# Kernel tuning notes

Measured on AMD Instinct MI355X. Metric: run time of the kernel, lower is better.

## Reference

```python
import jax, jax.numpy as jnp
import numpy as np

B, S, NX, NH = 2, 2048, 1024, 16
HD = NX // NH  # head dim = 64

def setup_inputs() -> dict:
    key = jax.random.key(0)
    k1, k2, k3 = jax.random.split(key, 3)
    return {
        "x": jax.random.normal(k1, (B, S, NX), dtype=jnp.float32),
        "c_attn_w": jax.random.normal(k2, (NX, 3 * NX), dtype=jnp.float32) * 0.02,
        "c_attn_b": jnp.zeros((3 * NX,), dtype=jnp.float32),
        "c_proj_w": jax.random.normal(k3, (NX, NX), dtype=jnp.float32) * 0.02,
        "c_proj_b": jnp.zeros((NX,), dtype=jnp.float32),
    }

def reference(x, c_attn_w, c_attn_b, c_proj_w, c_proj_b):
    b, s, nx = x.shape
    # fused QKV projection (Conv1D == affine on last dim)
    qkv = x @ c_attn_w + c_attn_b                      # [b, s, 3*nx]
    q, k, v = jnp.split(qkv, 3, axis=-1)
    # split heads -> [b, h, s, d]
    q = q.reshape(b, s, NH, HD).transpose(0, 2, 1, 3)
    k = k.reshape(b, s, NH, HD).transpose(0, 2, 1, 3)
    v = v.reshape(b, s, NH, HD).transpose(0, 2, 1, 3)
    # scaled scores with causal mask (masked_fill -1e10, matching original)
    w = jnp.einsum("bhqd,bhkd->bhqk", q, k) / jnp.sqrt(jnp.float32(HD))
    causal = jnp.tril(jnp.ones((s, s), dtype=bool))    # [s, s]
    w = jnp.where(causal[None, None, :, :], w, jnp.float32(-1e10))
    w = jax.nn.softmax(w, axis=-1)
    a = jnp.einsum("bhqk,bhkd->bhqd", w, v)            # [b, h, s, d]
    # merge heads
    a = a.transpose(0, 2, 1, 3).reshape(b, s, nx)
    # output projection (dropout is identity in eval)
    return a @ c_proj_w + c_proj_b
```

## Files before the change

kernel.cpp:

```cpp
#include <hip/hip_runtime.h>
#include <cstdint>

typedef unsigned short u16;
typedef unsigned int u32;
typedef float f32x4 __attribute__((ext_vector_type(4)));
typedef __bf16 bf16x8 __attribute__((ext_vector_type(8)));
typedef __bf16 bf16x4 __attribute__((ext_vector_type(4)));
typedef u16 u16x8 __attribute__((ext_vector_type(8)));

#define B_ 2
#define S_ 2048
#define NX_ 1024
#define NH_ 16
#define HD_ 64
#define T3_ 3072
#define M_ 4096
#define SCL 0.18033688011112042f

__device__ __forceinline__ u16 bfbits(float f) {
    __bf16 h = (__bf16)f;
    return __builtin_bit_cast(u16, h);
}

__device__ __forceinline__ void gload_lds16(const void* g, void* l) {
    auto gp = reinterpret_cast<const __attribute__((address_space(1))) u32*>(
        reinterpret_cast<uintptr_t>(g));
    auto lp = reinterpret_cast<__attribute__((address_space(3))) u32*>(
        reinterpret_cast<uintptr_t>(l));
    __builtin_amdgcn_global_load_lds(gp, lp, 16, 0, 0);
}

__global__ __launch_bounds__(256) void cvt_bf16_kernel(const float* __restrict__ X,
                                                       u16* __restrict__ Y) {
    int i = (blockIdx.x * 256 + threadIdx.x) * 4;
    float4 v = *reinterpret_cast<const float4*>(X + i);
    bf16x4 o;
    o[0] = (__bf16)v.x; o[1] = (__bf16)v.y; o[2] = (__bf16)v.z; o[3] = (__bf16)v.w;
    *reinterpret_cast<bf16x4*>(Y + i) = o;
}

__global__ __launch_bounds__(256) void transpose_cvt_kernel(const float* __restrict__ W,
                                                            u16* __restrict__ WT,
                                                            int K, int N) {
    __shared__ float tile[32][33];
    int nbx = N >> 5;
    int nb = (blockIdx.x % nbx) << 5;
    int kb = (blockIdx.x / nbx) << 5;
    int tx = threadIdx.x & 31, ty = threadIdx.x >> 5;
#pragma unroll
    for (int i = 0; i < 32; i += 8)
        tile[ty + i][tx] = W[(size_t)(kb + ty + i) * N + nb + tx];
    __syncthreads();
#pragma unroll
    for (int i = 0; i < 32; i += 8)
        WT[(size_t)(nb + ty + i) * K + kb + tx] = bfbits(tile[tx][ty + i]);
}

#define BM 128
#define BN 128
#define BK 64
__global__ __launch_bounds__(256) void gemm_bt_kernel(const u16* __restrict__ A,
                                                      const u16* __restrict__ Bt,
                                                      const float* __restrict__ bias,
                                                      u16* __restrict__ Cb,
                                                      float* __restrict__ Cf,
                                                      u16* __restrict__ Vt,
                                                      int vcol0, int qcols,
                                                      int M, int N, int K) {
    __shared__ u16 a_lds[2][BM * BK];
    __shared__ u16 b_lds[2][BN * BK];
    int nbn = N / BN;
    int nwg = gridDim.x;
    int orig = blockIdx.x;
    int wg = (orig & 7) * (nwg >> 3) + (orig >> 3);
    int bm = wg / nbn, bn = wg % nbn;
    int t = threadIdx.x;
    int w = t >> 6, l = t & 63, lg = l >> 4, lr = l & 15;
    int wr = w >> 1, wc = w & 1;
    const u16* Abase = A + (size_t)bm * BM * K;
    const u16* Bbase = Bt + (size_t)bn * BN * K;

    f32x4 zero4 = {0.f, 0.f, 0.f, 0.f};
    f32x4 acc[4][4];
#pragma unroll
    for (int m = 0; m < 4; ++m)
#pragma unroll
        for (int n = 0; n < 4; ++n) acc[m][n] = zero4;

    auto stage = [&](int kt, int bs) {
#pragma unroll
        for (int it = 0; it < 4; ++it) {
            int idx = it * 256 + t;
            int row = idx >> 3, ck = idx & 7;
            int cds = ck ^ (row & 7);
            int ubase = (it * 256 + w * 64) * 8;
            gload_lds16(Abase + (size_t)row * K + kt * BK + cds * 8, &a_lds[bs][ubase]);
            gload_lds16(Bbase + (size_t)row * K + kt * BK + cds * 8, &b_lds[bs][ubase]);
        }
    };

    stage(0, 0);
    __syncthreads();

    int nkt = K / BK;
    for (int kt = 0; kt < nkt; ++kt) {
        int cur = kt & 1;
        if (kt + 1 < nkt) stage(kt + 1, cur ^ 1);

#pragma unroll
        for (int ks = 0; ks < 2; ++ks) {
            int ck = (ks * 4 + lg) ^ (lr & 7);
            bf16x8 af[4], bf[4];
#pragma unroll
            for (int m = 0; m < 4; ++m)
                af[m] = *reinterpret_cast<const bf16x8*>(
                    &a_lds[cur][(wr * 64 + m * 16 + lr) * BK + ck * 8]);
#pragma unroll
            for (int n = 0; n < 4; ++n)
                bf[n] = *reinterpret_cast<const bf16x8*>(
                    &b_lds[cur][(wc * 64 + n * 16 + lr) * BK + ck * 8]);
            __builtin_amdgcn_s_setprio(1);
#pragma unroll
            for (int m = 0; m < 4; ++m)
#pragma unroll
                for (int n = 0; n < 4; ++n)
                    acc[m][n] = __builtin_amdgcn_mfma_f32_16x16x32_bf16(
                        af[m], bf[n], acc[m][n], 0, 0, 0);
            __builtin_amdgcn_s_setprio(0);
        }
        __syncthreads();
    }

#pragma unroll
    for (int n = 0; n < 4; ++n) {
        int col0 = bn * BN + wc * 64 + n * 16;
        int col = col0 + lr;
        float bv = bias[col];
        float sc = (col0 < qcols) ? SCL : 1.0f;
        bool isv = (Vt != nullptr) && (col0 >= vcol0);
#pragma unroll
        for (int m = 0; m < 4; ++m) {
            int row0 = bm * BM + wr * 64 + m * 16 + lg * 4;
            if (isv) {
                int nv = col - vcol0, hh = nv >> 6, dd = nv & 63;
                int bb = row0 >> 11, ss = row0 & 2047;
                bf16x4 pk;
#pragma unroll
                for (int r = 0; r < 4; ++r) pk[r] = (__bf16)(acc[m][n][r] + bv);
                *reinterpret_cast<bf16x4*>(
                    Vt + (((size_t)(bb * 16 + hh) * 64 + dd) << 11) + ss) = pk;
            } else {
#pragma unroll
                for (int r = 0; r < 4; ++r) {
                    float v = (acc[m][n][r] + bv) * sc;
                    if (Cf) Cf[(size_t)(row0 + r) * N + col] = v;
                    else    Cb[(size_t)(row0 + r) * N + col] = bfbits(v);
                }
            }
        }
    }
}

__global__ __launch_bounds__(512) void attn_kernel(const u16* __restrict__ qkv,
                                                   const u16* __restrict__ Vt,
                                                   u16* __restrict__ outa) {
    __shared__ u16 k_lds[2][4096];
    __shared__ u16 v_lds[2][4096];
    __shared__ u16 p_lds[8192];

    int bid = blockIdx.x;
    int g = bid & 31;
    int j = bid >> 5;
    int qt = (j < 8) ? (15 - j) : (j - 8);
    int b = g >> 4, h = g & 15;
    int t = threadIdx.x, w = t >> 6, l = t & 63, lg = l >> 4, lr = l & 15;
    const u16* base = qkv + (size_t)b * S_ * T3_;
    const u16* vbase = Vt + (size_t)g * 64 * S_;
    int prow = w * 16 + lr;
    int qb = qt * 128;
    int qrow = qb + w * 16 + lr;

    int srow = w * 8 + (l >> 3);
    auto stage = [&](int kt2, int bs) {
        int kb2 = kt2 * 64;
        int ckg = (l & 7) ^ (srow & 7);
        gload_lds16(base + (size_t)(kb2 + srow) * T3_ + NX_ + h * 64 + ckg * 8,
                    &k_lds[bs][w * 512]);
        gload_lds16(vbase + (size_t)srow * S_ + kb2 + ckg * 8,
                    &v_lds[bs][w * 512]);
    };

    f32x4 zero4 = {0.f, 0.f, 0.f, 0.f};

    bf16x8 qf[2];
#pragma unroll
    for (int ks = 0; ks < 2; ++ks)
        qf[ks] = *reinterpret_cast<const bf16x8*>(
            base + (size_t)qrow * T3_ + h * 64 + ks * 32 + lg * 8);

    f32x4 oacc[4];
#pragma unroll
    for (int dc = 0; dc < 4; ++dc) oacc[dc] = zero4;
    float mrun = -1e30f, lrun = 0.f;
    int nkt = 2 * qt + 2;
    int tw = 2 * qt + (w >> 2);

    stage(0, 0);
    __syncthreads();

    for (int kt = 0; kt < nkt; ++kt) {
        int cur = kt & 1;
        if (kt + 1 < nkt) stage(kt + 1, cur ^ 1);

        if (kt <= tw) {
            int kb = kt * 64;
            f32x4 sacc[4];
#pragma unroll
            for (int kn = 0; kn < 4; ++kn) sacc[kn] = zero4;
            __builtin_amdgcn_s_setprio(1);
#pragma unroll
            for (int ks = 0; ks < 2; ++ks) {
#pragma unroll
                for (int kn = 0; kn < 4; ++kn) {
                    bf16x8 kf = *reinterpret_cast<const bf16x8*>(
                        &k_lds[cur][(kn * 16 + lr) * 64 + (((ks * 4 + lg) ^ (lr & 7)) * 8)]);
                    sacc[kn] = __builtin_amdgcn_mfma_f32_16x16x32_bf16(
                        kf, qf[ks], sacc[kn], 0, 0, 0);
                }
            }
            __builtin_amdgcn_s_setprio(0);

            if (kt == tw) {
#pragma unroll
                for (int kn = 0; kn < 4; ++kn)
#pragma unroll
                    for (int r = 0; r < 4; ++r)
                        if (kb + kn * 16 + lg * 4 + r > qrow) sacc[kn][r] = -1e30f;
            }

            float mx = -1e30f;
#pragma unroll
            for (int kn = 0; kn < 4; ++kn) {
                float a0 = fmaxf(sacc[kn][0], sacc[kn][1]);
                float a1 = fmaxf(sacc[kn][2], sacc[kn][3]);
                mx = fmaxf(mx, fmaxf(a0, a1));
            }
            mx = fmaxf(mx, __shfl_xor(mx, 16));
            mx = fmaxf(mx, __shfl_xor(mx, 32));

            bool noresc = __all(mx <= mrun + 1.5f);
            float mnew = noresc ? mrun : fmaxf(mrun, mx);

            float rs = 0.f;
#pragma unroll
            for (int kn = 0; kn < 4; ++kn)
#pragma unroll
                for (int r = 0; r < 4; ++r) {
                    float pv = exp2f(sacc[kn][r] - mnew);
                    sacc[kn][r] = pv;
                    rs += pv;
                }
            rs += __shfl_xor(rs, 16);
            rs += __shfl_xor(rs, 32);

            if (noresc) {
                lrun += rs;
            } else {
                float fsc = exp2f(mrun - mnew);
                mrun = mnew;
                lrun = lrun * fsc + rs;
                float f0 = __shfl(fsc, lg * 4 + 0);
                float f1 = __shfl(fsc, lg * 4 + 1);
                float f2 = __shfl(fsc, lg * 4 + 2);
                float f3 = __shfl(fsc, lg * 4 + 3);
#pragma unroll
                for (int dc = 0; dc < 4; ++dc) {
                    oacc[dc][0] *= f0; oacc[dc][1] *= f1;
                    oacc[dc][2] *= f2; oacc[dc][3] *= f3;
                }
            }

#pragma unroll
            for (int kn = 0; kn < 4; ++kn) {
                bf16x4 pb;
                pb[0] = (__bf16)sacc[kn][0]; pb[1] = (__bf16)sacc[kn][1];
                pb[2] = (__bf16)sacc[kn][2]; pb[3] = (__bf16)sacc[kn][3];
                int byteoff = prow * 128 + (((2 * kn + (lg >> 1)) ^ (prow & 7)) * 16) + (lg & 1) * 8;
                *reinterpret_cast<bf16x4*>(reinterpret_cast<char*>(p_lds) + byteoff) = pb;
            }

            __builtin_amdgcn_s_setprio(1);
#pragma unroll
            for (int ks = 0; ks < 2; ++ks) {
                bf16x8 pf = *reinterpret_cast<const bf16x8*>(
                    reinterpret_cast<char*>(p_lds) + prow * 128 + (((ks * 4 + lg) ^ (prow & 7)) * 16));
#pragma unroll
                for (int dc = 0; dc < 4; ++dc) {
                    bf16x8 vf = *reinterpret_cast<const bf16x8*>(
                        &v_lds[cur][(dc * 16 + lr) * 64 + (((ks * 4 + lg) ^ (lr & 7)) * 8)]);
                    oacc[dc] = __builtin_amdgcn_mfma_f32_16x16x32_bf16(
                        pf, vf, oacc[dc], 0, 0, 0);
                }
            }
            __builtin_amdgcn_s_setprio(0);
        }
        __syncthreads();
    }

    float inv = 1.f / lrun;
    float i0 = __shfl(inv, lg * 4 + 0);
    float i1 = __shfl(inv, lg * 4 + 1);
    float i2 = __shfl(inv, lg * 4 + 2);
    float i3 = __shfl(inv, lg * 4 + 3);
    u16* ob = outa + (size_t)b * S_ * NX_;
#pragma unroll
    for (int r = 0; r < 4; ++r) {
        float ir = (r == 0) ? i0 : (r == 1) ? i1 : (r == 2) ? i2 : i3;
        int row = qb + w * 16 + lg * 4 + r;
#pragma unroll
        for (int dc = 0; dc < 4; ++dc)
            ob[(size_t)row * NX_ + h * 64 + dc * 16 + lr] = bfbits(oacc[dc][r] * ir);
    }
}

extern "C" void kernel_launch(void* const* d_in, const int* in_sizes, int n_in,
                              void* d_out, int out_size, void* d_ws, size_t ws_size,
                              hipStream_t stream) {
    const float* x        = (const float*)d_in[0];
    const float* c_attn_w = (const float*)d_in[1];
    const float* c_attn_b = (const float*)d_in[2];
    const float* c_proj_w = (const float*)d_in[3];
    const float* c_proj_b = (const float*)d_in[4];
    float* out = (float*)d_out;

    u16* xb     = (u16*)d_ws;
    u16* wqkvT  = xb + (size_t)M_ * NX_;
    u16* wprojT = wqkvT + (size_t)T3_ * NX_;
    u16* qkv    = wprojT + (size_t)NX_ * NX_;
    u16* attno  = xb;
    u16* Vtp    = (u16*)d_out;

    cvt_bf16_kernel<<<(M_ * NX_) / 1024, 256, 0, stream>>>(x, xb);
    transpose_cvt_kernel<<<(T3_ / 32) * (NX_ / 32), 256, 0, stream>>>(c_attn_w, wqkvT, NX_, T3_);
    transpose_cvt_kernel<<<(NX_ / 32) * (NX_ / 32), 256, 0, stream>>>(c_proj_w, wprojT, NX_, NX_);
    gemm_bt_kernel<<<(M_ / BM) * (T3_ / BN), 256, 0, stream>>>(
        xb, wqkvT, c_attn_b, qkv, nullptr, Vtp, 2 * NX_, NX_, M_, T3_, NX_);
    attn_kernel<<<512, 512, 0, stream>>>(qkv, Vtp, attno);
    gemm_bt_kernel<<<(M_ / BM) * (NX_ / BN), 256, 0, stream>>>(
        attno, wprojT, c_proj_b, nullptr, out, nullptr, 0, 0, M_, NX_, NX_);
}
```

Measured before the change: 120.1 us.

## Split attention KV range across two workgroups and merge partials; XCD-aware GEMM tile mapping

Each query tile's causal key range is now split into two halves handled by separate workgroups, so the attention grid doubles to 1024 blocks. Each half writes unnormalized bf16 partial outputs plus running max and sum, and a new merge kernel rescales and combines them. The aim is more parallelism and better balance on the long causal tiles. The cost is an extra kernel launch, extra memory traffic for partials and stats, and some precision loss from storing unnormalized partials in bf16. The GEMM block-to-tile mapping is also reworked to group tiles per XCD into 2D sub-grids for cache locality.

```diff
diff --git a/kernel.cpp b/kernel.cpp
--- a/kernel.cpp
+++ b/kernel.cpp
@@ -66,14 +66,14 @@
                                                       float* __restrict__ Cf,
                                                       u16* __restrict__ Vt,
                                                       int vcol0, int qcols,
+                                                      int gx, int sbm, int sbn,
                                                       int M, int N, int K) {
     __shared__ u16 a_lds[2][BM * BK];
     __shared__ u16 b_lds[2][BN * BK];
-    int nbn = N / BN;
-    int nwg = gridDim.x;
     int orig = blockIdx.x;
-    int wg = (orig & 7) * (nwg >> 3) + (orig >> 3);
-    int bm = wg / nbn, bn = wg % nbn;
+    int xcd = orig & 7, li = orig >> 3;
+    int bm = (xcd % gx) * sbm + li / sbn;
+    int bn = (xcd / gx) * sbn + li % sbn;
     int t = threadIdx.x;
     int w = t >> 6, l = t & 63, lg = l >> 4, lr = l & 15;
     int wr = w >> 1, wc = w & 1;
@@ -163,7 +163,9 @@
 
 __global__ __launch_bounds__(512) void attn_kernel(const u16* __restrict__ qkv,
                                                    const u16* __restrict__ Vt,
-                                                   u16* __restrict__ outa) {
+                                                   u16* __restrict__ part0,
+                                                   u16* __restrict__ part1,
+                                                   float* __restrict__ mlb) {
     __shared__ u16 k_lds[2][4096];
     __shared__ u16 v_lds[2][4096];
     __shared__ u16 p_lds[8192];
@@ -171,7 +173,8 @@
     int bid = blockIdx.x;
     int g = bid & 31;
     int j = bid >> 5;
-    int qt = (j < 8) ? (15 - j) : (j - 8);
+    int qt = 15 - (j >> 1);
+    int s = j & 1;
     int b = g >> 4, h = g & 15;
     int t = threadIdx.x, w = t >> 6, l = t & 63, lg = l >> 4, lr = l & 15;
     const u16* base = qkv + (size_t)b * S_ * T3_;
@@ -179,6 +182,10 @@
     int prow = w * 16 + lr;
     int qb = qt * 128;
     int qrow = qb + w * 16 + lr;
+
+    int tw = 2 * qt + (w >> 2);
+    int k0 = s ? (qt + 1) : 0;
+    int k1 = s ? (2 * qt + 2) : (qt + 1);
 
     int srow = w * 8 + (l >> 3);
     auto stage = [&](int kt2, int bs) {
@@ -202,15 +209,13 @@
 #pragma unroll
     for (int dc = 0; dc < 4; ++dc) oacc[dc] = zero4;
     float mrun = -1e30f, lrun = 0.f;
-    int nkt = 2 * qt + 2;
-    int tw = 2 * qt + (w >> 2);
-
-    stage(0, 0);
+
+    stage(k0, 0);
     __syncthreads();
 
-    for (int kt = 0; kt < nkt; ++kt) {
-        int cur = kt & 1;
-        if (kt + 1 < nkt) stage(kt + 1, cur ^ 1);
+    for (int kt = k0; kt < k1; ++kt) {
+        int cur = (kt - k0) & 1;
+        if (kt + 1 < k1) stage(kt + 1, cur ^ 1);
 
         if (kt <= tw) {
             int kb = kt * 64;
@@ -307,19 +312,42 @@
         __syncthreads();
     }
 
-    float inv = 1.f / lrun;
-    float i0 = __shfl(inv, lg * 4 + 0);
-    float i1 = __shfl(inv, lg * 4 + 1);
-    float i2 = __shfl(inv, lg * 4 + 2);
-    float i3 = __shfl(inv, lg * 4 + 3);
-    u16* ob = outa + (size_t)b * S_ * NX_;
+    u16* pb = (s ? part1 : part0) + (size_t)b * S_ * NX_;
 #pragma unroll
     for (int r = 0; r < 4; ++r) {
-        float ir = (r == 0) ? i0 : (r == 1) ? i1 : (r == 2) ? i2 : i3;
         int row = qb + w * 16 + lg * 4 + r;
 #pragma unroll
         for (int dc = 0; dc < 4; ++dc)
-            ob[(size_t)row * NX_ + h * 64 + dc * 16 + lr] = bfbits(oacc[dc][r] * ir);
+            pb[(size_t)row * NX_ + h * 64 + dc * 16 + lr] = bfbits(oacc[dc][r]);
+    }
+    if (lg == 0) {
+        float* f = mlb + (size_t)(b * S_ + qrow) * (T3_ / 2) + NX_ + h * 4 + s * 2;
+        f[0] = mrun; f[1] = lrun;
+    }
+}
+
+__global__ __launch_bounds__(256) void merge_kernel(u16* __restrict__ part0,
+                                                    const u16* __restrict__ part1,
+                                                    const float* __restrict__ mlb) {
+    int idx = blockIdx.x * 256 + threadIdx.x;
+    int tok = idx >> 4, h = idx & 15;
+    const float* f = mlb + (size_t)tok * (T3_ / 2) + NX_ + h * 4;
+    float m0 = f[0], l0 = f[1], m1 = f[2], l1 = f[3];
+    float M = fmaxf(m0, m1);
+    float e0 = exp2f(m0 - M), e1 = exp2f(m1 - M);
+    float inv = 1.f / (l0 * e0 + l1 * e1);
+    float a = e0 * inv, c = e1 * inv;
+    u16* p0 = part0 + (size_t)tok * NX_ + h * 64;
+    const u16* p1 = part1 + (size_t)tok * NX_ + h * 64;
+#pragma unroll
+    for (int i = 0; i < 8; ++i) {
+        bf16x8 v0 = *reinterpret_cast<const bf16x8*>(p0 + i * 8);
+        bf16x8 v1 = *reinterpret_cast<const bf16x8*>(p1 + i * 8);
+        bf16x8 o;
+#pragma unroll
+        for (int k = 0; k < 8; ++k)
+            o[k] = (__bf16)((float)v0[k] * a + (float)v1[k] * c);
+        *reinterpret_cast<bf16x8*>(p0 + i * 8) = o;
     }
 }
 
@@ -339,13 +367,16 @@
     u16* qkv    = wprojT + (size_t)NX_ * NX_;
     u16* attno  = xb;
     u16* Vtp    = (u16*)d_out;
+    u16* part1  = Vtp + (size_t)32 * 64 * S_;
+    float* mlb  = (float*)qkv;
 
     cvt_bf16_kernel<<<(M_ * NX_) / 1024, 256, 0, stream>>>(x, xb);
     transpose_cvt_kernel<<<(T3_ / 32) * (NX_ / 32), 256, 0, stream>>>(c_attn_w, wqkvT, NX_, T3_);
     transpose_cvt_kernel<<<(NX_ / 32) * (NX_ / 32), 256, 0, stream>>>(c_proj_w, wprojT, NX_, NX_);
     gemm_bt_kernel<<<(M_ / BM) * (T3_ / BN), 256, 0, stream>>>(
-        xb, wqkvT, c_attn_b, qkv, nullptr, Vtp, 2 * NX_, NX_, M_, T3_, NX_);
-    attn_kernel<<<512, 512, 0, stream>>>(qkv, Vtp, attno);
+        xb, wqkvT, c_attn_b, qkv, nullptr, Vtp, 2 * NX_, NX_, 4, 8, 12, M_, T3_, NX_);
+    attn_kernel<<<1024, 512, 0, stream>>>(qkv, Vtp, attno, part1, mlb);
+    merge_kernel<<<(M_ * NH_) / 256, 256, 0, stream>>>(attno, part1, mlb);
     gemm_bt_kernel<<<(M_ / BM) * (NX_ / BN), 256, 0, stream>>>(
-        attno, wprojT, c_proj_b, nullptr, out, nullptr, 0, 0, M_, NX_, NX_);
-}
+        attno, wprojT, c_proj_b, nullptr, out, nullptr, 0, 0, 4, 8, 4, M_, NX_, NX_);
+}
```

After: 120.8 us. Within noise of the previous version (+0.6%).
